# Optimization experiments

Measured on AMD Instinct MI355X. Metric: run time of the kernel, lower is better.

## Reference

```python
import jax, jax.numpy as jnp
import numpy as np

B, S, D0, H, K, C = 128, 64, 768, 256, 7, 3
EPS = 1e-12


def setup_inputs() -> dict:
    key = jax.random.key(0)
    ks = jax.random.split(key, 8)
    return {
        "premise": jax.random.normal(ks[0], (B, S, D0), jnp.float32),
        "hypothesis": jax.random.normal(ks[1], (B, S, D0), jnp.float32),
        "aW1": jax.random.normal(ks[2], (S, D0), jnp.float32) * 0.02,
        "conv1_w": jax.random.normal(ks[3], (D0, K, 2, H), jnp.float32) * 0.02,
        "conv1_b": jnp.full((H,), 1e-4, jnp.float32),
        "aW2": jax.random.normal(ks[4], (S, H), jnp.float32) * 0.02,
        "conv2_w": jax.random.normal(ks[5], (H, K, 2, H), jnp.float32) * 0.02,
        "conv2_b": jnp.full((H,), 1e-4, jnp.float32),
        "out_w": jax.random.normal(ks[6], (3, C), jnp.float32) * 0.1,
        "out_b": jnp.zeros((C,), jnp.float32),
    }


def _att_mat(x1, x2):
    # x1, x2: [B, d, W]; euclidean pairwise-distance attention 1/(1+||x1_i - x2_j||)
    n1 = jnp.sum(x1 * x1, axis=1)                       # [B, W]
    n2 = jnp.sum(x2 * x2, axis=1)                       # [B, W]
    dot = jnp.einsum('bdi,bdj->bij', x1, x2)            # [B, W, W]
    sq = jnp.maximum(n1[:, :, None] + n2[:, None, :] - 2.0 * dot, 0.0)
    return 1.0 / (1.0 + jnp.sqrt(sq + EPS))


def _cos_sim(v1, v2):
    n1 = jnp.sqrt(jnp.sum(v1 * v1, axis=1))
    n2 = jnp.sqrt(jnp.sum(v2 * v2, axis=1))
    return jnp.sum(v1 * v2, axis=1) / (n1 * n2 + EPS)


def _cnn_layer(x1, x2, aW, cw, cb):
    # x1, x2: [B, d, S]; aW: [S, d]; cw: [d, K, 2, H] (HWIO); cb: [H]
    att = _att_mat(x1, x2)                              # [B, S, S]
    # x1_a = (att @ aW)^T, x2_a = (att^T @ aW)^T  ->  [B, d, S]
    x1a = jnp.einsum('bij,jd->bdi', att, aW)
    x2a = jnp.einsum('bji,jd->bdi', att, aW)

    def conv(x, xa):
        xin = jnp.stack([x, xa], axis=-1)               # [B, d, S, 2] NHWC
        xin = jnp.pad(xin, ((0, 0), (0, 0), (K - 1, K - 1), (0, 0)))
        y = jax.lax.conv_general_dilated(
            xin, cw, window_strides=(1, 1), padding='VALID',
            dimension_numbers=('NHWC', 'HWIO', 'NHWC'))  # [B, 1, S+K-1, H]
        return jnp.transpose(jnp.tanh(y + cb)[:, 0], (0, 2, 1))  # [B, H, S+K-1]

    lc = conv(x1, x1a)
    rc = conv(x2, x2a)

    att2 = _att_mat(lc, rc)                             # [B, S+K-1, S+K-1]
    la = jnp.sum(att2, axis=2)                          # [B, S+K-1]
    ra = jnp.sum(att2, axis=1)                          # [B, S+K-1]

    def w_pool(x, a):
        # attention-weighted sliding-window sum of width K -> [B, H, S]
        w = x * a[:, None, :]
        return sum(w[:, :, j:j + S] for j in range(K))

    lwp = w_pool(lc, la)
    rwp = w_pool(rc, ra)
    lap = jnp.mean(lc, axis=2)                          # all-pool -> [B, H]
    rap = jnp.mean(rc, axis=2)
    return lwp, lap, rwp, rap


def _forward(premise, hypothesis, aW1, conv1_w, conv1_b, aW2, conv2_w, conv2_b,
             out_w, out_b):
    x1 = jnp.transpose(premise, (0, 2, 1))              # [B, D0, S]
    x2 = jnp.transpose(hypothesis, (0, 2, 1))
    LO0 = jnp.mean(x1, axis=2)                          # [B, D0]
    RO0 = jnp.mean(x2, axis=2)
    LI1, LO1, RI1, RO1 = _cnn_layer(x1, x2, aW1, conv1_w, conv1_b)
    _, LO2, _, RO2 = _cnn_layer(LI1, RI1, aW2, conv2_w, conv2_b)
    sims = jnp.stack(
        [_cos_sim(LO0, RO0), _cos_sim(LO1, RO1), _cos_sim(LO2, RO2)], axis=1)
    return sims @ out_w + out_b                         # logits [B, C]


def reference(premise, hypothesis, aW1, conv1_w, conv1_b, aW2, conv2_w,
              conv2_b, out_w, out_b):
    return _forward(premise, hypothesis, aW1, conv1_w, conv1_b, aW2, conv2_w,
                    conv2_b, out_w, out_b)
```

## Files before the change

### kernel.cpp

```cpp
#include <hip/hip_runtime.h>
#include <math.h>

typedef _Float16 f16;
typedef _Float16 half8 __attribute__((ext_vector_type(8)));
typedef _Float16 half4 __attribute__((ext_vector_type(4)));
typedef float floatx4 __attribute__((ext_vector_type(4)));

constexpr int B   = 128;
constexpr int S   = 64;
constexpr int D0  = 768;
constexpr int H   = 256;
constexpr int KW  = 7;
constexpr int NC  = 3;
constexpr int T70 = S + KW - 1;
constexpr float EPSF = 1e-12f;
constexpr int KTOT1 = ((D0 / 64) * 7 + 7) * 64;
constexpr int KTOT2 = ((H  / 64) * 7 + 7) * 64;

__device__ __forceinline__ void gload16(const void* g, void* l) {
  __builtin_amdgcn_global_load_lds(
      (const __attribute__((address_space(1))) unsigned int*)g,
      (__attribute__((address_space(3))) unsigned int*)l, 16, 0, 0);
}

__global__ __launch_bounds__(256) void k_cvtmean(const float* __restrict__ in0,
                                                 const float* __restrict__ in1,
                                                 f16* __restrict__ oh0,
                                                 f16* __restrict__ oh1,
                                                 float* __restrict__ mn0,
                                                 float* __restrict__ mn1) {
  constexpr int D4 = D0 / 4;
  const int side = blockIdx.y;
  const float* __restrict__ in = side ? in1 : in0;
  f16* __restrict__ outh = side ? oh1 : oh0;
  float* __restrict__ mean = side ? mn1 : mn0;
  const int idx = blockIdx.x * 256 + threadIdx.x;
  const int b = idx / D4, f4 = idx % D4;
  const float4* __restrict__ src = reinterpret_cast<const float4*>(in) + (size_t)b * S * D4 + f4;
  half4* __restrict__ dst = reinterpret_cast<half4*>(outh) + (size_t)b * S * D4 + f4;
  float4 acc = {0.f, 0.f, 0.f, 0.f};
  for (int t = 0; t < S; ++t) {
    float4 v = src[(size_t)t * D4];
    acc.x += v.x; acc.y += v.y; acc.z += v.z; acc.w += v.w;
    half4 o = {(f16)v.x, (f16)v.y, (f16)v.z, (f16)v.w};
    dst[(size_t)t * D4] = o;
  }
  const float inv = 1.f / S;
  mean[(size_t)b * D0 + f4 * 4 + 0] = acc.x * inv;
  mean[(size_t)b * D0 + f4 * 4 + 1] = acc.y * inv;
  mean[(size_t)b * D0 + f4 * 4 + 2] = acc.z * inv;
  mean[(size_t)b * D0 + f4 * 4 + 3] = acc.w * inv;
}

__device__ __forceinline__ void trw_x_dev(const float* __restrict__ cw,
                                          f16* __restrict__ Weff,
                                          int DPC, int Ktot, int t,
                                          f16 (*tile)[65]) {
  const int nb = DPC / 64;
  const int k = t / (nb * 4);
  const int rem = t % (nb * 4);
  const int h0 = (rem / nb) * 64, dd0 = (rem % nb) * 64;
  const int tx = threadIdx.x & 63, ty = threadIdx.x >> 6;
#pragma unroll
  for (int i = 0; i < 64; i += 4) {
    int dd = dd0 + i + ty;
    tile[i + ty][tx] = (f16)cw[(size_t)((dd * KW + k) * 2 + 0) * H + h0 + tx];
  }
  __syncthreads();
  const int sbase = ((dd0 >> 6) * 7 + k) * 64;
#pragma unroll
  for (int i = 0; i < 64; i += 4) {
    int h = h0 + i + ty;
    int col = sbase + (((tx >> 3) ^ (h & 7)) << 3) + (tx & 7);
    Weff[(size_t)h * Ktot + col] = tile[tx][i + ty];
  }
}

__device__ __forceinline__ void vgemm_dev(const float* __restrict__ aW,
                                          const float* __restrict__ cw,
                                          f16* __restrict__ Weff,
                                          int D, int Ktot, int t,
                                          half8* As, half8* Bs) {
  const int kk = t % 7;
  const int h0 = (t / 7) * 64;
  const int tid = threadIdx.x;
  const int lane = tid & 63, wave = tid >> 6;
  const int wr = wave >> 1, wc = wave & 1;
  const int l15 = lane & 15, g = lane >> 4;

  floatx4 acc[2][2];
#pragma unroll
  for (int i = 0; i < 2; ++i)
#pragma unroll
    for (int j = 0; j < 2; ++j) acc[i][j] = (floatx4)0.f;

  for (int k0 = 0; k0 < D; k0 += 32) {
    __syncthreads();
    {
      const int r = tid >> 2, cch = tid & 3;
      const float4* s = reinterpret_cast<const float4*>(aW + (size_t)r * D + k0 + cch * 8);
      float4 v0 = s[0], v1 = s[1];
      half8 hv = {(f16)v0.x, (f16)v0.y, (f16)v0.z, (f16)v0.w,
                  (f16)v1.x, (f16)v1.y, (f16)v1.z, (f16)v1.w};
      As[r * 4 + (cch ^ ((r >> 1) & 3))] = hv;
      const int hrow = tid & 63, kc = tid >> 6;
      half8 bv;
#pragma unroll
      for (int e = 0; e < 8; ++e) {
        const int d = k0 + kc * 8 + e;
        bv[e] = (f16)cw[(size_t)((d * KW + kk) * 2 + 1) * H + h0 + hrow];
      }
      Bs[hrow * 4 + (kc ^ ((hrow >> 1) & 3))] = bv;
    }
    __syncthreads();
    half8 af[2], bf[2];
#pragma unroll
    for (int fi = 0; fi < 2; ++fi) {
      const int row = wr * 32 + fi * 16 + l15;
      af[fi] = As[row * 4 + (g ^ ((row >> 1) & 3))];
    }
#pragma unroll
    for (int fj = 0; fj < 2; ++fj) {
      const int row = wc * 32 + fj * 16 + l15;
      bf[fj] = Bs[row * 4 + (g ^ ((row >> 1) & 3))];
    }
#pragma unroll
    for (int fi = 0; fi < 2; ++fi)
#pragma unroll
      for (int fj = 0; fj < 2; ++fj)
        acc[fi][fj] = __builtin_amdgcn_mfma_f32_16x16x32_f16(af[fi], bf[fj], acc[fi][fj], 0, 0, 0);
  }
  const int base = ((D / 64) * 7 + kk) * 64;
#pragma unroll
  for (int fi = 0; fi < 2; ++fi)
#pragma unroll
    for (int fj = 0; fj < 2; ++fj)
#pragma unroll
      for (int r = 0; r < 4; ++r) {
        const int j = wr * 32 + fi * 16 + g * 4 + r;
        const int h = h0 + wc * 32 + fj * 16 + l15;
        const int col = base + (((j >> 3) ^ (h & 7)) << 3) + (j & 7);
        Weff[(size_t)h * Ktot + col] = (f16)acc[fi][fj][r];
      }
}

__global__ __launch_bounds__(256) void k_wprep(const float* __restrict__ cw1,
                                               const float* __restrict__ aW1,
                                               f16* __restrict__ Weff1,
                                               const float* __restrict__ cw2,
                                               const float* __restrict__ aW2,
                                               f16* __restrict__ Weff2) {
  __shared__ f16 tile[64][65];
  __shared__ half8 As[64 * 4];
  __shared__ half8 Bs[64 * 4];
  const int bid = blockIdx.x;
  if (bid < 336)        trw_x_dev(cw1, Weff1, D0, KTOT1, bid, tile);
  else if (bid < 364)   vgemm_dev(aW1, cw1, Weff1, D0, KTOT1, bid - 336, As, Bs);
  else if (bid < 476)   trw_x_dev(cw2, Weff2, H, KTOT2, bid - 364, tile);
  else                  vgemm_dev(aW2, cw2, Weff2, H, KTOT2, bid - 476, As, Bs);
}

template<int D>
__global__ __launch_bounds__(256) void k_attst(const f16* __restrict__ X1,
                                               const f16* __restrict__ X2,
                                               f16* __restrict__ attA,
                                               f16* __restrict__ attT) {
  __shared__ half8 As[64 * 4];
  __shared__ half8 Bs[64 * 4];
  __shared__ float n1s[64], n2s[64];
  __shared__ half8 atA[64 * 8];
  __shared__ half8 atT[64 * 8];

  const int b = blockIdx.x, tid = threadIdx.x;
  const int lane = tid & 63, wave = tid >> 6;
  const int wr = wave >> 1, wc = wave & 1;
  const int l15 = lane & 15, g = lane >> 4;
  const f16* __restrict__ x1 = X1 + (size_t)b * S * D;
  const f16* __restrict__ x2 = X2 + (size_t)b * S * D;

  floatx4 acc[2][2];
#pragma unroll
  for (int i = 0; i < 2; ++i)
#pragma unroll
    for (int j = 0; j < 2; ++j) acc[i][j] = (floatx4)0.f;
  float na1 = 0.f, na2 = 0.f;

  for (int k0 = 0; k0 < D; k0 += 32) {
    __syncthreads();
    {
      const int r = tid >> 2, c = tid & 3;
      const int p = r * 4 + (c ^ ((r >> 1) & 3));
      As[p] = *reinterpret_cast<const half8*>(x1 + (size_t)r * D + k0 + c * 8);
      Bs[p] = *reinterpret_cast<const half8*>(x2 + (size_t)r * D + k0 + c * 8);
    }
    __syncthreads();
    half8 af[2], bf[2];
#pragma unroll
    for (int fi = 0; fi < 2; ++fi) {
      const int row = wr * 32 + fi * 16 + l15;
      af[fi] = As[row * 4 + (g ^ ((row >> 1) & 3))];
    }
#pragma unroll
    for (int fj = 0; fj < 2; ++fj) {
      const int row = wc * 32 + fj * 16 + l15;
      bf[fj] = Bs[row * 4 + (g ^ ((row >> 1) & 3))];
    }
#pragma unroll
    for (int fi = 0; fi < 2; ++fi)
#pragma unroll
      for (int fj = 0; fj < 2; ++fj)
        acc[fi][fj] = __builtin_amdgcn_mfma_f32_16x16x32_f16(af[fi], bf[fj], acc[fi][fj], 0, 0, 0);
    if (tid < 64) {
      const int r = tid;
#pragma unroll
      for (int c = 0; c < 4; ++c) {
        half8 v = As[r * 4 + (c ^ ((r >> 1) & 3))];
#pragma unroll
        for (int e = 0; e < 8; ++e) { float f = (float)v[e]; na1 = fmaf(f, f, na1); }
      }
    } else if (tid >= 128 && tid < 192) {
      const int r = tid - 128;
#pragma unroll
      for (int c = 0; c < 4; ++c) {
        half8 v = Bs[r * 4 + (c ^ ((r >> 1) & 3))];
#pragma unroll
        for (int e = 0; e < 8; ++e) { float f = (float)v[e]; na2 = fmaf(f, f, na2); }
      }
    }
  }
  if (tid < 64) n1s[tid] = na1;
  if (tid >= 128 && tid < 192) n2s[tid - 128] = na2;
  __syncthreads();

  f16* atAe = reinterpret_cast<f16*>(atA);
  f16* atTe = reinterpret_cast<f16*>(atT);
#pragma unroll
  for (int fi = 0; fi < 2; ++fi)
#pragma unroll
    for (int fj = 0; fj < 2; ++fj)
#pragma unroll
      for (int r = 0; r < 4; ++r) {
        const int i = wr * 32 + fi * 16 + g * 4 + r;
        const int j = wc * 32 + fj * 16 + l15;
        float sq = fmaxf(n1s[i] + n2s[j] - 2.f * acc[fi][fj][r], 0.f);
        const f16 v = (f16)(1.f / (1.f + sqrtf(sq + EPSF)));
        atAe[(i * 8 + ((j >> 3) ^ (i & 7))) * 8 + (j & 7)] = v;
        atTe[(j * 8 + ((i >> 3) ^ (j & 7))) * 8 + (i & 7)] = v;
      }
  __syncthreads();
  half8* Ag = reinterpret_cast<half8*>(attA) + (size_t)b * 512;
  half8* Tg = reinterpret_cast<half8*>(attT) + (size_t)b * 512;
  for (int idx = tid; idx < 512; idx += 256) {
    const int i = idx >> 3, ch = idx & 7;
    Ag[idx] = atA[i * 8 + (ch ^ (i & 7))];
    Tg[idx] = atT[i * 8 + (ch ^ (i & 7))];
  }
}

template<int DPC>
__global__ __launch_bounds__(256) void k_conv(const f16* __restrict__ X0,
                                              const f16* __restrict__ X1v,
                                              const f16* __restrict__ At0,
                                              const f16* __restrict__ At1,
                                              const f16* __restrict__ Weff,
                                              const float* __restrict__ bias,
                                              f16* __restrict__ O16_0,
                                              f16* __restrict__ O16_1) {
  constexpr int NDQX = DPC / 64;
  constexpr int NX7 = NDQX * 7;
  constexpr int NSTEP = NX7 + 7;
  constexpr int KTOT = NSTEP * 64;
  __shared__ half8 Wl[70 * 8];
  __shared__ half8 B8[2][128 * 8];

  const int tid = threadIdx.x;
  const int bid = blockIdx.x;
  const int xcd = bid & 7, slot = bid >> 3;
  const int n0 = (xcd >> 2) * 128;
  const int w = slot * 4 + (xcd & 3);
  const int z = w & 1, mblk = w >> 1;
  const int m0 = mblk * 64;
  const f16* __restrict__ Xs  = z ? X1v : X0;
  const f16* __restrict__ Ats = z ? At1 : At0;
  f16* __restrict__ Out16 = z ? O16_1 : O16_0;

  const int lane = tid & 63, wave = tid >> 6;
  const int wr = wave >> 1, wc = wave & 1;
  const int l15 = lane & 15, g = lane >> 4;
  const int r0 = tid >> 3, c8 = tid & 7;

  int jr[3] = {r0, r0 + 32, 64 + r0};
  int aoffX[3], aoffA[3];
  bool aval[3];
#pragma unroll
  for (int p = 0; p < 3; ++p) {
    const int u = m0 - 6 + jr[p];
    const int uc = u < 0 ? 0 : u;
    const int bn = uc / T70;
    const int tl = uc - bn * T70;
    aval[p] = (u >= 0) && (tl < S);
    aoffX[p] = (bn * S + tl) * DPC + c8 * 8;
    aoffA[p] = (bn * 64 + tl) * 64 + c8 * 8;
  }
  const bool has2 = (r0 < 6);
  const int bchunk0 = wave * 64 + lane;
  const f16* __restrict__ bsrc = Weff + (size_t)n0 * KTOT;

  floatx4 acc[2][4];
#pragma unroll
  for (int i = 0; i < 2; ++i)
#pragma unroll
    for (int j = 0; j < 4; ++j) acc[i][j] = (floatx4)0.f;

  half8 rA[3];
  auto aLoad = [&](const f16* __restrict__ src, const int* aoff, int co) {
#pragma unroll
    for (int p = 0; p < 2; ++p)
      rA[p] = aval[p] ? *reinterpret_cast<const half8*>(src + aoff[p] + co)
                      : (half8)(f16)0.f;
    if (has2)
      rA[2] = aval[2] ? *reinterpret_cast<const half8*>(src + aoff[2] + co)
                      : (half8)(f16)0.f;
  };
  auto aWrite = [&]() {
#pragma unroll
    for (int p = 0; p < 2; ++p) {
      const int j = jr[p];
      Wl[j * 8 + (c8 ^ (j & 7))] = rA[p];
    }
    if (has2) {
      const int j = jr[2];
      Wl[j * 8 + (c8 ^ (j & 7))] = rA[2];
    }
  };
  auto bStage = [&](int buf, int ks) {
    const int o = ks * 64;
#pragma unroll
    for (int q = 0; q < 4; ++q) {
      const int chunk = q * 256 + bchunk0;
      const int r = chunk >> 3, cc = chunk & 7;
      gload16(bsrc + (size_t)r * KTOT + o + cc * 8, &B8[buf][q * 256 + wave * 64]);
    }
  };
  auto compute = [&](int ks) {
    const int k = (ks < NX7) ? (ks % 7) : (ks - NX7);
    const int buf = ks & 1;
    half8 af[2][2], bf[4][2];
#pragma unroll
    for (int i = 0; i < 2; ++i) {
      const int j = wr * 32 + i * 16 + l15 + k;
#pragma unroll
      for (int s = 0; s < 2; ++s)
        af[i][s] = Wl[j * 8 + ((s * 4 + g) ^ (j & 7))];
    }
#pragma unroll
    for (int jx = 0; jx < 4; ++jx) {
      const int row = wc * 64 + jx * 16 + l15;
#pragma unroll
      for (int s = 0; s < 2; ++s)
        bf[jx][s] = B8[buf][row * 8 + ((s * 4 + g) ^ (row & 7))];
    }
#pragma unroll
    for (int s = 0; s < 2; ++s)
#pragma unroll
      for (int i = 0; i < 2; ++i)
#pragma unroll
        for (int jx = 0; jx < 4; ++jx)
          acc[i][jx] = __builtin_amdgcn_mfma_f32_16x16x32_f16(af[i][s], bf[jx][s], acc[i][jx], 0, 0, 0);
  };

  bStage(0, 0);
  aLoad(Xs, aoffX, 0);
  aWrite();
  __syncthreads();

  for (int ks = 0; ks < NSTEP; ++ks) {
    const int nxt = ks + 1;
    const bool more = nxt < NSTEP;
    if (more) {
      bStage(nxt & 1, nxt);
      if (ks % 7 == 5) {
        const int wnd = ks / 7 + 1;
        if (wnd < NDQX) aLoad(Xs, aoffX, wnd * 64);
        else if (wnd == NDQX) aLoad(Ats, aoffA, 0);
      }
    }
    compute(ks);
    if (more && (nxt % 7 == 0)) { __syncthreads(); aWrite(); }
    __syncthreads();
  }

#pragma unroll
  for (int i = 0; i < 2; ++i) {
    const int mr = m0 + wr * 32 + i * 16 + g * 4;
#pragma unroll
    for (int jx = 0; jx < 4; ++jx) {
      const int h = n0 + wc * 64 + jx * 16 + l15;
      const float bv = bias[h];
#pragma unroll
      for (int r = 0; r < 4; ++r)
        Out16[(size_t)(mr + r) * H + h] = (f16)tanhf(acc[i][jx][r] + bv);
    }
  }
}

__global__ __launch_bounds__(256) void k_pool(const f16* __restrict__ lcTh,
                                              const f16* __restrict__ rcTh,
                                              float* __restrict__ LO1,
                                              float* __restrict__ RO1,
                                              f16* __restrict__ LI1h,
                                              f16* __restrict__ RI1h) {
  constexpr int W = T70, WP = 96, D = H;
  constexpr int FR = WP / 32;
  __shared__ half8 As[WP * 4];
  __shared__ half8 Bs[WP * 4];
  __shared__ float n1s[WP], n2s[WP];
  __shared__ float att_s[WP * (WP + 1)];
  __shared__ float la_s[W], ra_s[W];

  const int b = blockIdx.x, tid = threadIdx.x;
  const int lane = tid & 63, wave = tid >> 6;
  const int wr = wave >> 1, wc = wave & 1;
  const int l15 = lane & 15, g = lane >> 4;
  const f16* __restrict__ x1 = lcTh + (size_t)b * W * D;
  const f16* __restrict__ x2 = rcTh + (size_t)b * W * D;

  floatx4 acc[FR][FR];
#pragma unroll
  for (int i = 0; i < FR; ++i)
#pragma unroll
    for (int j = 0; j < FR; ++j) acc[i][j] = (floatx4)0.f;
  float na1 = 0.f, na2 = 0.f;

  for (int k0 = 0; k0 < D; k0 += 32) {
    __syncthreads();
    for (int u = tid; u < WP * 4; u += 256) {
      const int r = u >> 2, c = u & 3;
      half8 v1 = (half8)(f16)0.f, v2 = (half8)(f16)0.f;
      if (r < W) {
        v1 = *reinterpret_cast<const half8*>(x1 + (size_t)r * D + k0 + c * 8);
        v2 = *reinterpret_cast<const half8*>(x2 + (size_t)r * D + k0 + c * 8);
      }
      const int p = r * 4 + (c ^ ((r >> 1) & 3));
      As[p] = v1;
      Bs[p] = v2;
    }
    __syncthreads();
    half8 af[FR], bf[FR];
#pragma unroll
    for (int fi = 0; fi < FR; ++fi) {
      const int row = wr * 16 * FR + fi * 16 + l15;
      af[fi] = As[row * 4 + (g ^ ((row >> 1) & 3))];
    }
#pragma unroll
    for (int fj = 0; fj < FR; ++fj) {
      const int row = wc * 16 * FR + fj * 16 + l15;
      bf[fj] = Bs[row * 4 + (g ^ ((row >> 1) & 3))];
    }
#pragma unroll
    for (int fi = 0; fi < FR; ++fi)
#pragma unroll
      for (int fj = 0; fj < FR; ++fj)
        acc[fi][fj] = __builtin_amdgcn_mfma_f32_16x16x32_f16(af[fi], bf[fj], acc[fi][fj], 0, 0, 0);
    if (tid < WP) {
      const int r = tid;
#pragma unroll
      for (int c = 0; c < 4; ++c) {
        half8 v = As[r * 4 + (c ^ ((r >> 1) & 3))];
#pragma unroll
        for (int e = 0; e < 8; ++e) { float f = (float)v[e]; na1 = fmaf(f, f, na1); }
      }
    } else if (tid >= 128 && tid < 128 + WP) {
      const int r = tid - 128;
#pragma unroll
      for (int c = 0; c < 4; ++c) {
        half8 v = Bs[r * 4 + (c ^ ((r >> 1) & 3))];
#pragma unroll
        for (int e = 0; e < 8; ++e) { float f = (float)v[e]; na2 = fmaf(f, f, na2); }
      }
    }
  }
  if (tid < WP) n1s[tid] = na1;
  if (tid >= 128 && tid < 128 + WP) n2s[tid - 128] = na2;
  __syncthreads();

#pragma unroll
  for (int fi = 0; fi < FR; ++fi)
#pragma unroll
    for (int fj = 0; fj < FR; ++fj)
#pragma unroll
      for (int r = 0; r < 4; ++r) {
        const int i = wr * 16 * FR + fi * 16 + g * 4 + r;
        const int j = wc * 16 * FR + fj * 16 + l15;
        if (i < W && j < W) {
          float sq = fmaxf(n1s[i] + n2s[j] - 2.f * acc[fi][fj][r], 0.f);
          att_s[i * (WP + 1) + j] = 1.f / (1.f + sqrtf(sq + EPSF));
        }
      }
  __syncthreads();
  if (tid < W) {
    float sum = 0.f;
    for (int j = 0; j < W; ++j) sum += att_s[tid * (WP + 1) + j];
    la_s[tid] = sum;
  }
  if (tid >= 128 && tid < 128 + W) {
    const int j = tid - 128;
    float sum = 0.f;
    for (int i = 0; i < W; ++i) sum += att_s[i * (WP + 1) + j];
    ra_s[j] = sum;
  }
  __syncthreads();

  f16 (*wv)[H] = reinterpret_cast<f16(*)[H]>(att_s);
  const int h = tid;
#pragma unroll
  for (int side = 0; side < 2; ++side) {
    const f16* __restrict__ xc = (side ? rcTh : lcTh) + (size_t)b * T70 * H;
    const float* __restrict__ av = side ? ra_s : la_s;
    float* __restrict__ LO = side ? RO1 : LO1;
    f16* __restrict__ LI = (side ? RI1h : LI1h) + (size_t)b * S * H;
    __syncthreads();
    float sum = 0.f;
    for (int t = 0; t < T70; ++t) {
      const float v = (float)xc[(size_t)t * H + h];
      sum += v;
      wv[t][h] = (f16)(v * av[t]);
    }
    LO[(size_t)b * H + h] = sum * (1.f / T70);
    __syncthreads();
    for (int s = 0; s < S; ++s) {
      float a = 0.f;
#pragma unroll
      for (int j = 0; j < KW; ++j) a += (float)wv[s + j][h];
      LI[(size_t)s * H + h] = (f16)a;
    }
  }
}

__global__ __launch_bounds__(256) void k_final(const float* __restrict__ LO0,
                                               const float* __restrict__ RO0,
                                               const float* __restrict__ LO1,
                                               const float* __restrict__ RO1,
                                               const f16* __restrict__ lcTh,
                                               const f16* __restrict__ rcTh,
                                               const float* __restrict__ out_w,
                                               const float* __restrict__ out_b,
                                               float* __restrict__ out) {
  const int b = blockIdx.x;
  const int tid = threadIdx.x;
  __shared__ float red[3][4];
  __shared__ float sims[3];

  float lo2 = 0.f, ro2 = 0.f;
  {
    const f16* lp = lcTh + (size_t)b * T70 * H + tid;
    const f16* rp = rcTh + (size_t)b * T70 * H + tid;
    for (int t = 0; t < T70; ++t) {
      lo2 += (float)lp[(size_t)t * H];
      ro2 += (float)rp[(size_t)t * H];
    }
    lo2 *= (1.f / T70);
    ro2 *= (1.f / T70);
  }

  const float* Ls[2] = {LO0 + (size_t)b * D0, LO1 + (size_t)b * H};
  const float* Rs[2] = {RO0 + (size_t)b * D0, RO1 + (size_t)b * H};
  const int dims[2] = {D0, H};
#pragma unroll
  for (int p = 0; p < 3; ++p) {
    float dot, q1, q2;
    if (p < 2) {
      dot = 0.f; q1 = 0.f; q2 = 0.f;
      for (int i = tid; i < dims[p]; i += 256) {
        const float v1 = Ls[p][i], v2 = Rs[p][i];
        dot = fmaf(v1, v2, dot);
        q1  = fmaf(v1, v1, q1);
        q2  = fmaf(v2, v2, q2);
      }
    } else {
      dot = lo2 * ro2; q1 = lo2 * lo2; q2 = ro2 * ro2;
    }
#pragma unroll
    for (int off = 32; off > 0; off >>= 1) {
      dot += __shfl_down(dot, off);
      q1  += __shfl_down(q1, off);
      q2  += __shfl_down(q2, off);
    }
    if ((tid & 63) == 0) { red[0][tid >> 6] = dot; red[1][tid >> 6] = q1; red[2][tid >> 6] = q2; }
    __syncthreads();
    if (tid == 0) {
      float d = red[0][0] + red[0][1] + red[0][2] + red[0][3];
      float a = red[1][0] + red[1][1] + red[1][2] + red[1][3];
      float c = red[2][0] + red[2][1] + red[2][2] + red[2][3];
      sims[p] = d / (sqrtf(a) * sqrtf(c) + EPSF);
    }
    __syncthreads();
  }
  if (tid < NC) {
    float v = out_b[tid];
#pragma unroll
    for (int k = 0; k < 3; ++k) v = fmaf(sims[k], out_w[k * NC + tid], v);
    out[b * NC + tid] = v;
  }
}

extern "C" void kernel_launch(void* const* d_in, const int* in_sizes, int n_in,
                              void* d_out, int out_size, void* d_ws, size_t ws_size,
                              hipStream_t stream) {
  const float* premise    = (const float*)d_in[0];
  const float* hypothesis = (const float*)d_in[1];
  const float* aW1        = (const float*)d_in[2];
  const float* conv1_w    = (const float*)d_in[3];
  const float* conv1_b    = (const float*)d_in[4];
  const float* aW2        = (const float*)d_in[5];
  const float* conv2_w    = (const float*)d_in[6];
  const float* conv2_b    = (const float*)d_in[7];
  const float* out_w      = (const float*)d_in[8];
  const float* out_b      = (const float*)d_in[9];
  float* out = (float*)d_out;

  char* ws = (char*)d_ws;
  size_t off = 0;
  auto alloc = [&](size_t bytes) {
    void* p = ws + off;
    off += (bytes + 255) & ~(size_t)255;
    return p;
  };
  f16*   Weff1 = (f16*)alloc((size_t)H * KTOT1 * 2);
  f16*   Weff2 = (f16*)alloc((size_t)H * KTOT2 * 2);
  f16*   Xh    = (f16*)alloc((size_t)B * S * D0 * 2);
  f16*   Yh    = (f16*)alloc((size_t)B * S * D0 * 2);
  f16*   attA  = (f16*)alloc((size_t)B * S * S * 2);
  f16*   attT  = (f16*)alloc((size_t)B * S * S * 2);
  f16*   LI1h  = (f16*)alloc((size_t)B * S * H * 2);
  f16*   RI1h  = (f16*)alloc((size_t)B * S * H * 2);
  f16*   lcTh  = (f16*)alloc((size_t)B * T70 * H * 2);
  f16*   rcTh  = (f16*)alloc((size_t)B * T70 * H * 2);
  float* LO0   = (float*)alloc((size_t)B * D0 * 4);
  float* RO0   = (float*)alloc((size_t)B * D0 * 4);
  float* LO1   = (float*)alloc((size_t)B * H * 4);
  float* RO1   = (float*)alloc((size_t)B * H * 4);

  k_cvtmean<<<dim3(B * (D0 / 4) / 256, 2), 256, 0, stream>>>(premise, hypothesis, Xh, Yh, LO0, RO0);
  k_wprep<<<504, 256, 0, stream>>>(conv1_w, aW1, Weff1, conv2_w, aW2, Weff2);
  k_attst<D0><<<B, 256, 0, stream>>>(Xh, Yh, attA, attT);
  k_conv<D0><<<560, 256, 0, stream>>>(Xh, Yh, attA, attT, Weff1, conv1_b, lcTh, rcTh);
  k_pool<<<B, 256, 0, stream>>>(lcTh, rcTh, LO1, RO1, LI1h, RI1h);
  k_attst<H><<<B, 256, 0, stream>>>(LI1h, RI1h, attA, attT);
  k_conv<H><<<560, 256, 0, stream>>>(LI1h, RI1h, attA, attT, Weff2, conv2_b, lcTh, rcTh);
  k_final<<<B, 256, 0, stream>>>(LO0, RO0, LO1, RO1, lcTh, rcTh, out_w, out_b, out);
}
```

Measured before the change: 212.8 us.

## Merge cvtmean into weight-prep launch and fuse layer-2 attention into pool kernel

The input fp32-to-fp16 conversion and mean blocks now run in the same launch as the weight-preparation blocks, removing one kernel launch. The layer-2 attention computation (previously its own k_attst<H> launch) is folded into the tail of k_pool. Each block re-reads the LI1h/RI1h rows it just wrote, behind a threadfence and barrier, and emits attA/attT directly. This removes two launches and their gaps. The cost is a longer, serialized per-batch pool kernel with only 128 blocks, and it relies on reading back its own global writes.

```diff
diff --git a/kernel.cpp b/kernel.cpp
--- a/kernel.cpp
+++ b/kernel.cpp
@@ -23,18 +23,11 @@
       (__attribute__((address_space(3))) unsigned int*)l, 16, 0, 0);
 }
 
-__global__ __launch_bounds__(256) void k_cvtmean(const float* __restrict__ in0,
-                                                 const float* __restrict__ in1,
-                                                 f16* __restrict__ oh0,
-                                                 f16* __restrict__ oh1,
-                                                 float* __restrict__ mn0,
-                                                 float* __restrict__ mn1) {
+__device__ __forceinline__ void cvtmean_dev(const float* __restrict__ in,
+                                            f16* __restrict__ outh,
+                                            float* __restrict__ mean, int gx) {
   constexpr int D4 = D0 / 4;
-  const int side = blockIdx.y;
-  const float* __restrict__ in = side ? in1 : in0;
-  f16* __restrict__ outh = side ? oh1 : oh0;
-  float* __restrict__ mean = side ? mn1 : mn0;
-  const int idx = blockIdx.x * 256 + threadIdx.x;
+  const int idx = gx * 256 + threadIdx.x;
   const int b = idx / D4, f4 = idx % D4;
   const float4* __restrict__ src = reinterpret_cast<const float4*>(in) + (size_t)b * S * D4 + f4;
   half4* __restrict__ dst = reinterpret_cast<half4*>(outh) + (size_t)b * S * D4 + f4;
@@ -144,20 +137,31 @@
       }
 }
 
-__global__ __launch_bounds__(256) void k_wprep(const float* __restrict__ cw1,
-                                               const float* __restrict__ aW1,
-                                               f16* __restrict__ Weff1,
-                                               const float* __restrict__ cw2,
-                                               const float* __restrict__ aW2,
-                                               f16* __restrict__ Weff2) {
+__global__ __launch_bounds__(256) void k_pre(const float* __restrict__ premise,
+                                             const float* __restrict__ hypothesis,
+                                             f16* __restrict__ Xh,
+                                             f16* __restrict__ Yh,
+                                             float* __restrict__ LO0,
+                                             float* __restrict__ RO0,
+                                             const float* __restrict__ cw1,
+                                             const float* __restrict__ aW1,
+                                             f16* __restrict__ Weff1,
+                                             const float* __restrict__ cw2,
+                                             const float* __restrict__ aW2,
+                                             f16* __restrict__ Weff2) {
   __shared__ f16 tile[64][65];
   __shared__ half8 As[64 * 4];
   __shared__ half8 Bs[64 * 4];
   const int bid = blockIdx.x;
-  if (bid < 336)        trw_x_dev(cw1, Weff1, D0, KTOT1, bid, tile);
-  else if (bid < 364)   vgemm_dev(aW1, cw1, Weff1, D0, KTOT1, bid - 336, As, Bs);
-  else if (bid < 476)   trw_x_dev(cw2, Weff2, H, KTOT2, bid - 364, tile);
-  else                  vgemm_dev(aW2, cw2, Weff2, H, KTOT2, bid - 476, As, Bs);
+  if (bid < 96)        cvtmean_dev(premise,    Xh, LO0, bid);
+  else if (bid < 192)  cvtmean_dev(hypothesis, Yh, RO0, bid - 96);
+  else {
+    const int t = bid - 192;
+    if (t < 336)       trw_x_dev(cw1, Weff1, D0, KTOT1, t, tile);
+    else if (t < 364)  vgemm_dev(aW1, cw1, Weff1, D0, KTOT1, t - 336, As, Bs);
+    else if (t < 476)  trw_x_dev(cw2, Weff2, H, KTOT2, t - 364, tile);
+    else               vgemm_dev(aW2, cw2, Weff2, H, KTOT2, t - 476, As, Bs);
+  }
 }
 
 template<int D>
@@ -409,7 +413,9 @@
                                               float* __restrict__ LO1,
                                               float* __restrict__ RO1,
                                               f16* __restrict__ LI1h,
-                                              f16* __restrict__ RI1h) {
+                                              f16* __restrict__ RI1h,
+                                              f16* __restrict__ attA,
+                                              f16* __restrict__ attT) {
   constexpr int W = T70, WP = 96, D = H;
   constexpr int FR = WP / 32;
   __shared__ half8 As[WP * 4];
@@ -425,114 +431,205 @@
   const f16* __restrict__ x1 = lcTh + (size_t)b * W * D;
   const f16* __restrict__ x2 = rcTh + (size_t)b * W * D;
 
-  floatx4 acc[FR][FR];
-#pragma unroll
-  for (int i = 0; i < FR; ++i)
-#pragma unroll
-    for (int j = 0; j < FR; ++j) acc[i][j] = (floatx4)0.f;
-  float na1 = 0.f, na2 = 0.f;
-
-  for (int k0 = 0; k0 < D; k0 += 32) {
-    __syncthreads();
-    for (int u = tid; u < WP * 4; u += 256) {
-      const int r = u >> 2, c = u & 3;
-      half8 v1 = (half8)(f16)0.f, v2 = (half8)(f16)0.f;
-      if (r < W) {
-        v1 = *reinterpret_cast<const half8*>(x1 + (size_t)r * D + k0 + c * 8);
-        v2 = *reinterpret_cast<const half8*>(x2 + (size_t)r * D + k0 + c * 8);
-      }
-      const int p = r * 4 + (c ^ ((r >> 1) & 3));
-      As[p] = v1;
-      Bs[p] = v2;
-    }
-    __syncthreads();
-    half8 af[FR], bf[FR];
-#pragma unroll
-    for (int fi = 0; fi < FR; ++fi) {
-      const int row = wr * 16 * FR + fi * 16 + l15;
-      af[fi] = As[row * 4 + (g ^ ((row >> 1) & 3))];
-    }
-#pragma unroll
-    for (int fj = 0; fj < FR; ++fj) {
-      const int row = wc * 16 * FR + fj * 16 + l15;
-      bf[fj] = Bs[row * 4 + (g ^ ((row >> 1) & 3))];
-    }
+  {
+    floatx4 acc[FR][FR];
+#pragma unroll
+    for (int i = 0; i < FR; ++i)
+#pragma unroll
+      for (int j = 0; j < FR; ++j) acc[i][j] = (floatx4)0.f;
+    float na1 = 0.f, na2 = 0.f;
+
+    for (int k0 = 0; k0 < D; k0 += 32) {
+      __syncthreads();
+      for (int u = tid; u < WP * 4; u += 256) {
+        const int r = u >> 2, c = u & 3;
+        half8 v1 = (half8)(f16)0.f, v2 = (half8)(f16)0.f;
+        if (r < W) {
+          v1 = *reinterpret_cast<const half8*>(x1 + (size_t)r * D + k0 + c * 8);
+          v2 = *reinterpret_cast<const half8*>(x2 + (size_t)r * D + k0 + c * 8);
+        }
+        const int p = r * 4 + (c ^ ((r >> 1) & 3));
+        As[p] = v1;
+        Bs[p] = v2;
+      }
+      __syncthreads();
+      half8 af[FR], bf[FR];
+#pragma unroll
+      for (int fi = 0; fi < FR; ++fi) {
+        const int row = wr * 16 * FR + fi * 16 + l15;
+        af[fi] = As[row * 4 + (g ^ ((row >> 1) & 3))];
+      }
+#pragma unroll
+      for (int fj = 0; fj < FR; ++fj) {
+        const int row = wc * 16 * FR + fj * 16 + l15;
+        bf[fj] = Bs[row * 4 + (g ^ ((row >> 1) & 3))];
+      }
+#pragma unroll
+      for (int fi = 0; fi < FR; ++fi)
+#pragma unroll
+        for (int fj = 0; fj < FR; ++fj)
+          acc[fi][fj] = __builtin_amdgcn_mfma_f32_16x16x32_f16(af[fi], bf[fj], acc[fi][fj], 0, 0, 0);
+      if (tid < WP) {
+        const int r = tid;
+#pragma unroll
+        for (int c = 0; c < 4; ++c) {
+          half8 v = As[r * 4 + (c ^ ((r >> 1) & 3))];
+#pragma unroll
+          for (int e = 0; e < 8; ++e) { float f = (float)v[e]; na1 = fmaf(f, f, na1); }
+        }
+      } else if (tid >= 128 && tid < 128 + WP) {
+        const int r = tid - 128;
+#pragma unroll
+        for (int c = 0; c < 4; ++c) {
+          half8 v = Bs[r * 4 + (c ^ ((r >> 1) & 3))];
+#pragma unroll
+          for (int e = 0; e < 8; ++e) { float f = (float)v[e]; na2 = fmaf(f, f, na2); }
+        }
+      }
+    }
+    if (tid < WP) n1s[tid] = na1;
+    if (tid >= 128 && tid < 128 + WP) n2s[tid - 128] = na2;
+    __syncthreads();
+
 #pragma unroll
     for (int fi = 0; fi < FR; ++fi)
 #pragma unroll
       for (int fj = 0; fj < FR; ++fj)
-        acc[fi][fj] = __builtin_amdgcn_mfma_f32_16x16x32_f16(af[fi], bf[fj], acc[fi][fj], 0, 0, 0);
-    if (tid < WP) {
-      const int r = tid;
-#pragma unroll
-      for (int c = 0; c < 4; ++c) {
-        half8 v = As[r * 4 + (c ^ ((r >> 1) & 3))];
-#pragma unroll
-        for (int e = 0; e < 8; ++e) { float f = (float)v[e]; na1 = fmaf(f, f, na1); }
-      }
-    } else if (tid >= 128 && tid < 128 + WP) {
-      const int r = tid - 128;
-#pragma unroll
-      for (int c = 0; c < 4; ++c) {
-        half8 v = Bs[r * 4 + (c ^ ((r >> 1) & 3))];
-#pragma unroll
-        for (int e = 0; e < 8; ++e) { float f = (float)v[e]; na2 = fmaf(f, f, na2); }
-      }
-    }
-  }
-  if (tid < WP) n1s[tid] = na1;
-  if (tid >= 128 && tid < 128 + WP) n2s[tid - 128] = na2;
+#pragma unroll
+        for (int r = 0; r < 4; ++r) {
+          const int i = wr * 16 * FR + fi * 16 + g * 4 + r;
+          const int j = wc * 16 * FR + fj * 16 + l15;
+          if (i < W && j < W) {
+            float sq = fmaxf(n1s[i] + n2s[j] - 2.f * acc[fi][fj][r], 0.f);
+            att_s[i * (WP + 1) + j] = 1.f / (1.f + sqrtf(sq + EPSF));
+          }
+        }
+    __syncthreads();
+    if (tid < W) {
+      float sum = 0.f;
+      for (int j = 0; j < W; ++j) sum += att_s[tid * (WP + 1) + j];
+      la_s[tid] = sum;
+    }
+    if (tid >= 128 && tid < 128 + W) {
+      const int j = tid - 128;
+      float sum = 0.f;
+      for (int i = 0; i < W; ++i) sum += att_s[i * (WP + 1) + j];
+      ra_s[j] = sum;
+    }
+    __syncthreads();
+  }
+
+  {
+    f16 (*wv)[H] = reinterpret_cast<f16(*)[H]>(att_s);
+    const int h = tid;
+#pragma unroll
+    for (int side = 0; side < 2; ++side) {
+      const f16* __restrict__ xc = (side ? rcTh : lcTh) + (size_t)b * T70 * H;
+      const float* __restrict__ av = side ? ra_s : la_s;
+      float* __restrict__ LO = side ? RO1 : LO1;
+      f16* __restrict__ LI = (side ? RI1h : LI1h) + (size_t)b * S * H;
+      __syncthreads();
+      float sum = 0.f;
+      for (int t = 0; t < T70; ++t) {
+        const float v = (float)xc[(size_t)t * H + h];
+        sum += v;
+        wv[t][h] = (f16)(v * av[t]);
+      }
+      LO[(size_t)b * H + h] = sum * (1.f / T70);
+      __syncthreads();
+      for (int s = 0; s < S; ++s) {
+        float a = 0.f;
+#pragma unroll
+        for (int j = 0; j < KW; ++j) a += (float)wv[s + j][h];
+        LI[(size_t)s * H + h] = (f16)a;
+      }
+    }
+  }
+
+  __threadfence();
   __syncthreads();
 
-#pragma unroll
-  for (int fi = 0; fi < FR; ++fi)
-#pragma unroll
-    for (int fj = 0; fj < FR; ++fj)
-#pragma unroll
-      for (int r = 0; r < 4; ++r) {
-        const int i = wr * 16 * FR + fi * 16 + g * 4 + r;
-        const int j = wc * 16 * FR + fj * 16 + l15;
-        if (i < W && j < W) {
+  {
+    const f16* __restrict__ y1 = LI1h + (size_t)b * S * H;
+    const f16* __restrict__ y2 = RI1h + (size_t)b * S * H;
+    floatx4 acc[2][2];
+#pragma unroll
+    for (int i = 0; i < 2; ++i)
+#pragma unroll
+      for (int j = 0; j < 2; ++j) acc[i][j] = (floatx4)0.f;
+    float na1 = 0.f, na2 = 0.f;
+
+    for (int k0 = 0; k0 < H; k0 += 32) {
+      __syncthreads();
+      {
+        const int r = tid >> 2, c = tid & 3;
+        const int p = r * 4 + (c ^ ((r >> 1) & 3));
+        As[p] = *reinterpret_cast<const half8*>(y1 + (size_t)r * H + k0 + c * 8);
+        Bs[p] = *reinterpret_cast<const half8*>(y2 + (size_t)r * H + k0 + c * 8);
+      }
+      __syncthreads();
+      half8 af[2], bf[2];
+#pragma unroll
+      for (int fi = 0; fi < 2; ++fi) {
+        const int row = wr * 32 + fi * 16 + l15;
+        af[fi] = As[row * 4 + (g ^ ((row >> 1) & 3))];
+      }
+#pragma unroll
+      for (int fj = 0; fj < 2; ++fj) {
+        const int row = wc * 32 + fj * 16 + l15;
+        bf[fj] = Bs[row * 4 + (g ^ ((row >> 1) & 3))];
+      }
+#pragma unroll
+      for (int fi = 0; fi < 2; ++fi)
+#pragma unroll
+        for (int fj = 0; fj < 2; ++fj)
+          acc[fi][fj] = __builtin_amdgcn_mfma_f32_16x16x32_f16(af[fi], bf[fj], acc[fi][fj], 0, 0, 0);
+      if (tid < 64) {
+        const int r = tid;
+#pragma unroll
+        for (int c = 0; c < 4; ++c) {
+          half8 v = As[r * 4 + (c ^ ((r >> 1) & 3))];
+#pragma unroll
+          for (int e = 0; e < 8; ++e) { float f = (float)v[e]; na1 = fmaf(f, f, na1); }
+        }
+      } else if (tid >= 128 && tid < 192) {
+        const int r = tid - 128;
+#pragma unroll
+        for (int c = 0; c < 4; ++c) {
+          half8 v = Bs[r * 4 + (c ^ ((r >> 1) & 3))];
+#pragma unroll
+          for (int e = 0; e < 8; ++e) { float f = (float)v[e]; na2 = fmaf(f, f, na2); }
+        }
+      }
+    }
+    if (tid < 64) n1s[tid] = na1;
+    if (tid >= 128 && tid < 192) n2s[tid - 128] = na2;
+    __syncthreads();
+
+    half8* atA = reinterpret_cast<half8*>(att_s);
+    half8* atT = atA + 64 * 8;
+    f16* atAe = reinterpret_cast<f16*>(atA);
+    f16* atTe = reinterpret_cast<f16*>(atT);
+#pragma unroll
+    for (int fi = 0; fi < 2; ++fi)
+#pragma unroll
+      for (int fj = 0; fj < 2; ++fj)
+#pragma unroll
+        for (int r = 0; r < 4; ++r) {
+          const int i = wr * 32 + fi * 16 + g * 4 + r;
+          const int j = wc * 32 + fj * 16 + l15;
           float sq = fmaxf(n1s[i] + n2s[j] - 2.f * acc[fi][fj][r], 0.f);
-          att_s[i * (WP + 1) + j] = 1.f / (1.f + sqrtf(sq + EPSF));
+          const f16 v = (f16)(1.f / (1.f + sqrtf(sq + EPSF)));
+          atAe[(i * 8 + ((j >> 3) ^ (i & 7))) * 8 + (j & 7)] = v;
+          atTe[(j * 8 + ((i >> 3) ^ (j & 7))) * 8 + (i & 7)] = v;
         }
-      }
-  __syncthreads();
-  if (tid < W) {
-    float sum = 0.f;
-    for (int j = 0; j < W; ++j) sum += att_s[tid * (WP + 1) + j];
-    la_s[tid] = sum;
-  }
-  if (tid >= 128 && tid < 128 + W) {
-    const int j = tid - 128;
-    float sum = 0.f;
-    for (int i = 0; i < W; ++i) sum += att_s[i * (WP + 1) + j];
-    ra_s[j] = sum;
-  }
-  __syncthreads();
-
-  f16 (*wv)[H] = reinterpret_cast<f16(*)[H]>(att_s);
-  const int h = tid;
-#pragma unroll
-  for (int side = 0; side < 2; ++side) {
-    const f16* __restrict__ xc = (side ? rcTh : lcTh) + (size_t)b * T70 * H;
-    const float* __restrict__ av = side ? ra_s : la_s;
-    float* __restrict__ LO = side ? RO1 : LO1;
-    f16* __restrict__ LI = (side ? RI1h : LI1h) + (size_t)b * S * H;
-    __syncthreads();
-    float sum = 0.f;
-    for (int t = 0; t < T70; ++t) {
-      const float v = (float)xc[(size_t)t * H + h];
-      sum += v;
-      wv[t][h] = (f16)(v * av[t]);
-    }
-    LO[(size_t)b * H + h] = sum * (1.f / T70);
-    __syncthreads();
-    for (int s = 0; s < S; ++s) {
-      float a = 0.f;
-#pragma unroll
-      for (int j = 0; j < KW; ++j) a += (float)wv[s + j][h];
-      LI[(size_t)s * H + h] = (f16)a;
+    __syncthreads();
+    half8* Ag = reinterpret_cast<half8*>(attA) + (size_t)b * 512;
+    half8* Tg = reinterpret_cast<half8*>(attT) + (size_t)b * 512;
+    for (int idx = tid; idx < 512; idx += 256) {
+      const int i = idx >> 3, ch = idx & 7;
+      Ag[idx] = atA[i * 8 + (ch ^ (i & 7))];
+      Tg[idx] = atT[i * 8 + (ch ^ (i & 7))];
     }
   }
 }
@@ -641,12 +738,11 @@
   float* LO1   = (float*)alloc((size_t)B * H * 4);
   float* RO1   = (float*)alloc((size_t)B * H * 4);
 
-  k_cvtmean<<<dim3(B * (D0 / 4) / 256, 2), 256, 0, stream>>>(premise, hypothesis, Xh, Yh, LO0, RO0);
-  k_wprep<<<504, 256, 0, stream>>>(conv1_w, aW1, Weff1, conv2_w, aW2, Weff2);
+  k_pre<<<696, 256, 0, stream>>>(premise, hypothesis, Xh, Yh, LO0, RO0,
+                                 conv1_w, aW1, Weff1, conv2_w, aW2, Weff2);
   k_attst<D0><<<B, 256, 0, stream>>>(Xh, Yh, attA, attT);
   k_conv<D0><<<560, 256, 0, stream>>>(Xh, Yh, attA, attT, Weff1, conv1_b, lcTh, rcTh);
-  k_pool<<<B, 256, 0, stream>>>(lcTh, rcTh, LO1, RO1, LI1h, RI1h);
-  k_attst<H><<<B, 256, 0, stream>>>(LI1h, RI1h, attA, attT);
+  k_pool<<<B, 256, 0, stream>>>(lcTh, rcTh, LO1, RO1, LI1h, RI1h, attA, attT);
   k_conv<H><<<560, 256, 0, stream>>>(LI1h, RI1h, attA, attT, Weff2, conv2_b, lcTh, rcTh);
   k_final<<<B, 256, 0, stream>>>(LO0, RO0, LO1, RO1, lcTh, rcTh, out_w, out_b, out);
 }
```

New measurement: 214.3 us, median of 2. No clear change (+0.7%).
